# Optimization experiments

Hardware: AMD Instinct MI355X
Metric: run time of the kernel (lower is better)

Reference implementation:

```python
import jax, jax.numpy as jnp
import numpy as np

N, INSIZE, K, D = 512, 512, 64, 16


def setup_inputs() -> dict:
    key = jax.random.key(0)
    k1, k2, k3 = jax.random.split(key, 3)
    x = jax.random.normal(k1, (N, INSIZE), dtype=jnp.float32)
    W = jax.random.normal(k2, (K * D, INSIZE), dtype=jnp.float32) * (1.0 / np.sqrt(INSIZE))
    b = jax.random.normal(k3, (K * D,), dtype=jnp.float32) * 0.01
    return {"x": x, "W": W, "b": b}


def reference(x, W, b):
    # Linear: [N, insize] -> [N, K*D] -> [N, K, D]
    feat = (x @ W.T + b).reshape(-1, K, D)
    n = feat.shape[0]
    # Pairwise L1 distance over D: norm[i, k, j] = sum_d |feat[i,k,d] - feat[j,k,d]|
    # feature [N,K,D,1] vs feature_ [1,K,D,N] in the original broadcast
    diff = jnp.abs(feat[:, :, :, None] - jnp.transpose(feat, (1, 2, 0))[None])  # [N,K,D,N]
    norm = jnp.sum(diff, axis=2)  # [N,K,N]
    # Eraser: suppress self-similarity on the diagonal with a large penalty
    eraser = jnp.eye(n, dtype=feat.dtype)[:, None, :]  # [N,1,N]
    c_b = jnp.exp(-(norm + eraser * 1e6))
    o_b = jnp.sum(c_b, axis=2)  # [N,K]
    return jnp.concatenate((x, o_b), axis=1)  # [N, insize+K]
```

## Files before the change

kernel.cpp:

```cpp
#include <hip/hip_runtime.h>

#define NPTS 512
#define INS  512
#define KDIM 64
#define DDIM 16
#define CDIM (KDIM*DDIM)
#define OUTC (INS + KDIM)

typedef __attribute__((ext_vector_type(4))) float f32x4;
typedef __attribute__((ext_vector_type(8))) short short8v;
typedef __attribute__((ext_vector_type(4))) unsigned short u16x4;
typedef __attribute__((ext_vector_type(8))) unsigned short u16x8;

__device__ __forceinline__ float exp2_fast(float x) {
    return __builtin_amdgcn_exp2f(x);
}

__device__ __forceinline__ unsigned short f2bf_rne(float f) {
    unsigned u = __float_as_uint(f);
    u += 0x7FFF + ((u >> 16) & 1);
    return (unsigned short)(u >> 16);
}
__device__ __forceinline__ float bf2f(unsigned short h) {
    return __uint_as_float(((unsigned)h) << 16);
}

__global__ __launch_bounds__(256) void convert_kernel(
    const float* __restrict__ x, const float* __restrict__ W,
    unsigned short* __restrict__ xh, unsigned short* __restrict__ xl,
    unsigned short* __restrict__ wh, unsigned short* __restrict__ wl)
{
    const int gid = blockIdx.x * 256 + threadIdx.x;
    const float4* src;
    unsigned short *dh, *dl;
    int idx;
    if (gid < NPTS * INS / 4) {
        src = (const float4*)x; idx = gid; dh = xh; dl = xl;
    } else {
        src = (const float4*)W; idx = gid - NPTS * INS / 4; dh = wh; dl = wl;
    }
    float4 v = src[idx];
    u16x4 hv, lv;
    hv[0] = f2bf_rne(v.x); lv[0] = f2bf_rne(v.x - bf2f(hv[0]));
    hv[1] = f2bf_rne(v.y); lv[1] = f2bf_rne(v.y - bf2f(hv[1]));
    hv[2] = f2bf_rne(v.z); lv[2] = f2bf_rne(v.z - bf2f(hv[2]));
    hv[3] = f2bf_rne(v.w); lv[3] = f2bf_rne(v.w - bf2f(hv[3]));
    *(u16x4*)&dh[idx * 4] = hv;
    *(u16x4*)&dl[idx * 4] = lv;
}

#define BM 64
#define BN 64
#define BK 32
#define LDK 40

__global__ __launch_bounds__(256) void gemm_mfma_kernel(
    const unsigned short* __restrict__ xh, const unsigned short* __restrict__ xl,
    const unsigned short* __restrict__ wh, const unsigned short* __restrict__ wl,
    const float* __restrict__ bias,
    float* __restrict__ featT)
{
    __shared__ unsigned short Ah[BM * LDK], Al[BM * LDK];
    __shared__ unsigned short Bh[BN * LDK], Bl[BN * LDK];

    const int tid   = threadIdx.x;
    const int cbase = blockIdx.x * BN;
    const int ibase = blockIdx.y * BM;

    const int lane = tid & 63;
    const int wv   = tid >> 6;
    const int wm   = wv >> 1;
    const int wn   = wv & 1;

    const int srow = tid >> 2;
    const int skg  = tid & 3;
    const size_t gA0 = (size_t)(ibase + srow) * INS + skg * 8;
    const size_t gB0 = (size_t)(cbase + srow) * INS + skg * 8;
    const int    loff = srow * LDK + skg * 8;

    const int frow  = lane & 15;
    const int fg    = lane >> 4;
    const int aoff  = (wm * 32 + frow) * LDK + fg * 8;
    const int boff  = (wn * 32 + frow) * LDK + fg * 8;

    f32x4 acc[2][2] = {};

    u16x8 ra = *(const u16x8*)&xh[gA0];
    u16x8 rl = *(const u16x8*)&xl[gA0];
    u16x8 rb = *(const u16x8*)&wh[gB0];
    u16x8 rc = *(const u16x8*)&wl[gB0];

    for (int kt = 0; kt < INS / BK; ++kt) {
        __syncthreads();
        *(u16x8*)&Ah[loff] = ra;
        *(u16x8*)&Al[loff] = rl;
        *(u16x8*)&Bh[loff] = rb;
        *(u16x8*)&Bl[loff] = rc;
        __syncthreads();
        if (kt + 1 < INS / BK) {
            const size_t o = (size_t)(kt + 1) * BK;
            ra = *(const u16x8*)&xh[gA0 + o];
            rl = *(const u16x8*)&xl[gA0 + o];
            rb = *(const u16x8*)&wh[gB0 + o];
            rc = *(const u16x8*)&wl[gB0 + o];
        }

        short8v ah[2], al[2], bh[2], bl[2];
        #pragma unroll
        for (int f = 0; f < 2; ++f) {
            ah[f] = *(const short8v*)&Ah[aoff + f * 16 * LDK];
            al[f] = *(const short8v*)&Al[aoff + f * 16 * LDK];
            bh[f] = *(const short8v*)&Bh[boff + f * 16 * LDK];
            bl[f] = *(const short8v*)&Bl[boff + f * 16 * LDK];
        }
        #pragma unroll
        for (int m = 0; m < 2; ++m) {
            #pragma unroll
            for (int n = 0; n < 2; ++n) {
                acc[m][n] = __builtin_amdgcn_mfma_f32_16x16x32_bf16(ah[m], bh[n], acc[m][n], 0, 0, 0);
                acc[m][n] = __builtin_amdgcn_mfma_f32_16x16x32_bf16(ah[m], bl[n], acc[m][n], 0, 0, 0);
                acc[m][n] = __builtin_amdgcn_mfma_f32_16x16x32_bf16(al[m], bh[n], acc[m][n], 0, 0, 0);
            }
        }
    }

    const float LOG2E = 1.4426950408889634f;
    const int r0 = (lane >> 4) * 4;
    #pragma unroll
    for (int m = 0; m < 2; ++m) {
        const int i0 = ibase + wm * 32 + m * 16 + r0;
        #pragma unroll
        for (int n = 0; n < 2; ++n) {
            const int c  = cbase + wn * 32 + n * 16 + (lane & 15);
            const float bv = bias[c];
            const int kk = c >> 4;
            const int d  = c & 15;
            float* dst = featT + (size_t)kk * NPTS * DDIM + d;
            #pragma unroll
            for (int r = 0; r < 4; ++r) {
                dst[(size_t)(i0 + r) * DDIM] = (acc[m][n][r] + bv) * LOG2E;
            }
        }
    }
}

__global__ __launch_bounds__(256) void init_out_kernel(
    const float* __restrict__ x, float* __restrict__ out)
{
    const int idx = blockIdx.x * 256 + threadIdx.x;
    const int i  = idx / (OUTC / 4);
    const int j4 = idx - i * (OUTC / 4);
    float4 v;
    if (j4 < INS / 4) {
        v = ((const float4*)x)[i * (INS / 4) + j4];
    } else {
        v = make_float4(-1.0f, -1.0f, -1.0f, -1.0f);
    }
    ((float4*)out)[idx] = v;
}

__global__ __launch_bounds__(256, 4) void pairwise_kernel(
    const float* __restrict__ f0, float* __restrict__ out)
{
    const int k     = blockIdx.x;
    const int itile = blockIdx.y;
    const int jq    = blockIdx.z;

    __shared__ float fj[128 * DDIM];
    __shared__ float part[4][128];

    {
        const size_t base = ((size_t)k * NPTS + jq * 128) * DDIM;
        const float4* s0 = (const float4*)(f0 + base);
        float4* dst = (float4*)fj;
        dst[threadIdx.x]       = s0[threadIdx.x];
        dst[threadIdx.x + 256] = s0[threadIdx.x + 256];
    }

    const int lane = threadIdx.x & 63;
    const int wv   = threadIdx.x >> 6;
    const int i0   = itile * 128 + lane;
    const int i1   = i0 + 64;

    float fi0[16], fi1[16];
    {
        const float4* p0 = (const float4*)(f0 + ((size_t)k * NPTS + i0) * DDIM);
        const float4* p1 = (const float4*)(f0 + ((size_t)k * NPTS + i1) * DDIM);
        #pragma unroll
        for (int q = 0; q < 4; ++q) {
            float4 a = p0[q];
            fi0[q * 4 + 0] = a.x; fi0[q * 4 + 1] = a.y;
            fi0[q * 4 + 2] = a.z; fi0[q * 4 + 3] = a.w;
            float4 b = p1[q];
            fi1[q * 4 + 0] = b.x; fi1[q * 4 + 1] = b.y;
            fi1[q * 4 + 2] = b.z; fi1[q * 4 + 3] = b.w;
        }
    }
    __syncthreads();

    float acc0 = 0.f, acc1 = 0.f;
    const float* fp = fj + wv * 32 * DDIM;
    #pragma unroll 2
    for (int jj = 0; jj < 32; ++jj) {
        const float* p = fp + jj * DDIM;
        float4 q0 = *(const float4*)(p);
        float4 q1 = *(const float4*)(p + 4);
        float4 q2 = *(const float4*)(p + 8);
        float4 q3 = *(const float4*)(p + 12);
        {
            float a0 = fabsf(fi0[0]  - q0.x) + fabsf(fi0[1]  - q0.y)
                     + fabsf(fi0[2]  - q0.z) + fabsf(fi0[3]  - q0.w);
            float a1 = fabsf(fi0[4]  - q1.x) + fabsf(fi0[5]  - q1.y)
                     + fabsf(fi0[6]  - q1.z) + fabsf(fi0[7]  - q1.w);
            float a2 = fabsf(fi0[8]  - q2.x) + fabsf(fi0[9]  - q2.y)
                     + fabsf(fi0[10] - q2.z) + fabsf(fi0[11] - q2.w);
            float a3 = fabsf(fi0[12] - q3.x) + fabsf(fi0[13] - q3.y)
                     + fabsf(fi0[14] - q3.z) + fabsf(fi0[15] - q3.w);
            acc0 += exp2_fast(-((a0 + a1) + (a2 + a3)));
        }
        {
            float b0 = fabsf(fi1[0]  - q0.x) + fabsf(fi1[1]  - q0.y)
                     + fabsf(fi1[2]  - q0.z) + fabsf(fi1[3]  - q0.w);
            float b1 = fabsf(fi1[4]  - q1.x) + fabsf(fi1[5]  - q1.y)
                     + fabsf(fi1[6]  - q1.z) + fabsf(fi1[7]  - q1.w);
            float b2 = fabsf(fi1[8]  - q2.x) + fabsf(fi1[9]  - q2.y)
                     + fabsf(fi1[10] - q2.z) + fabsf(fi1[11] - q2.w);
            float b3 = fabsf(fi1[12] - q3.x) + fabsf(fi1[13] - q3.y)
                     + fabsf(fi1[14] - q3.z) + fabsf(fi1[15] - q3.w);
            acc1 += exp2_fast(-((b0 + b1) + (b2 + b3)));
        }
    }

    part[wv][lane]      = acc0;
    part[wv][lane + 64] = acc1;
    __syncthreads();

    if (threadIdx.x < 128) {
        float s = (part[0][threadIdx.x] + part[1][threadIdx.x])
                + (part[2][threadIdx.x] + part[3][threadIdx.x]);
        const int i = itile * 128 + threadIdx.x;
        atomicAdd(&out[(size_t)i * OUTC + INS + k], s);
    }
}

extern "C" void kernel_launch(void* const* d_in, const int* in_sizes, int n_in,
                              void* d_out, int out_size, void* d_ws, size_t ws_size,
                              hipStream_t stream) {
    const float* x    = (const float*)d_in[0];
    const float* W    = (const float*)d_in[1];
    const float* bias = (const float*)d_in[2];
    float* out = (float*)d_out;

    float* featT = (float*)d_ws;
    unsigned short* xh = (unsigned short*)((char*)d_ws + (size_t)(2 << 20));
    unsigned short* xl = xh + (size_t)NPTS * INS;
    unsigned short* wh = xl + (size_t)NPTS * INS;
    unsigned short* wl = wh + (size_t)CDIM * INS;

    convert_kernel<<<dim3((NPTS * INS / 4 + CDIM * INS / 4) / 256), 256, 0, stream>>>(
        x, W, xh, xl, wh, wl);
    gemm_mfma_kernel<<<dim3(CDIM / BN, NPTS / BM), 256, 0, stream>>>(
        xh, xl, wh, wl, bias, featT);
    init_out_kernel<<<dim3(NPTS * (OUTC / 4) / 256), 256, 0, stream>>>(x, out);
    pairwise_kernel<<<dim3(KDIM, 4, 4), 256, 0, stream>>>(featT, out);
}
```

Measured before the change: 94.77 us.

## Fuse output init into convert, halve GEMM M-tile, drop pairwise atomics

The x-to-output copy moves into the convert kernel as extra blocks, which removes the separate init kernel launch. The GEMM M-tile drops from 64 to 32 rows, doubling the block count to improve occupancy on a small problem. The pairwise kernel now uses 1024-thread blocks covering all 512 j-points and reads j-rows directly from global/L1 instead of staging them in LDS. Because each block now holds the full sum, it writes the result directly and subtracts the diagonal self term (1.0), replacing atomicAdd and the -1 initialization. The risk is heavier per-thread global reads in the inner loop and lower per-CU occupancy with the large blocks.

```diff
diff --git a/kernel.cpp b/kernel.cpp
--- a/kernel.cpp
+++ b/kernel.cpp
@@ -27,29 +27,39 @@
 
 __global__ __launch_bounds__(256) void convert_kernel(
     const float* __restrict__ x, const float* __restrict__ W,
+    float* __restrict__ out,
     unsigned short* __restrict__ xh, unsigned short* __restrict__ xl,
     unsigned short* __restrict__ wh, unsigned short* __restrict__ wl)
 {
-    const int gid = blockIdx.x * 256 + threadIdx.x;
-    const float4* src;
-    unsigned short *dh, *dl;
-    int idx;
-    if (gid < NPTS * INS / 4) {
-        src = (const float4*)x; idx = gid; dh = xh; dl = xl;
+    const int b = blockIdx.x;
+    const int tid = threadIdx.x;
+    if (b < 768) {
+        const int gid = b * 256 + tid;
+        const float4* src;
+        unsigned short *dh, *dl;
+        int idx;
+        if (gid < NPTS * INS / 4) {
+            src = (const float4*)x; idx = gid; dh = xh; dl = xl;
+        } else {
+            src = (const float4*)W; idx = gid - NPTS * INS / 4; dh = wh; dl = wl;
+        }
+        float4 v = src[idx];
+        u16x4 hv, lv;
+        hv[0] = f2bf_rne(v.x); lv[0] = f2bf_rne(v.x - bf2f(hv[0]));
+        hv[1] = f2bf_rne(v.y); lv[1] = f2bf_rne(v.y - bf2f(hv[1]));
+        hv[2] = f2bf_rne(v.z); lv[2] = f2bf_rne(v.z - bf2f(hv[2]));
+        hv[3] = f2bf_rne(v.w); lv[3] = f2bf_rne(v.w - bf2f(hv[3]));
+        *(u16x4*)&dh[idx * 4] = hv;
+        *(u16x4*)&dl[idx * 4] = lv;
     } else {
-        src = (const float4*)W; idx = gid - NPTS * INS / 4; dh = wh; dl = wl;
-    }
-    float4 v = src[idx];
-    u16x4 hv, lv;
-    hv[0] = f2bf_rne(v.x); lv[0] = f2bf_rne(v.x - bf2f(hv[0]));
-    hv[1] = f2bf_rne(v.y); lv[1] = f2bf_rne(v.y - bf2f(hv[1]));
-    hv[2] = f2bf_rne(v.z); lv[2] = f2bf_rne(v.z - bf2f(hv[2]));
-    hv[3] = f2bf_rne(v.w); lv[3] = f2bf_rne(v.w - bf2f(hv[3]));
-    *(u16x4*)&dh[idx * 4] = hv;
-    *(u16x4*)&dl[idx * 4] = lv;
-}
-
-#define BM 64
+        const int idx = (b - 768) * 256 + tid;
+        const int i  = idx >> 7;
+        const int j4 = idx & 127;
+        ((float4*)out)[i * (OUTC / 4) + j4] = ((const float4*)x)[i * (INS / 4) + j4];
+    }
+}
+
+#define BM 32
 #define BN 64
 #define BK 32
 #define LDK 40
@@ -72,120 +82,87 @@
     const int wm   = wv >> 1;
     const int wn   = wv & 1;
 
-    const int srow = tid >> 2;
-    const int skg  = tid & 3;
-    const size_t gA0 = (size_t)(ibase + srow) * INS + skg * 8;
-    const size_t gB0 = (size_t)(cbase + srow) * INS + skg * 8;
-    const int    loff = srow * LDK + skg * 8;
-
-    const int frow  = lane & 15;
-    const int fg    = lane >> 4;
-    const int aoff  = (wm * 32 + frow) * LDK + fg * 8;
-    const int boff  = (wn * 32 + frow) * LDK + fg * 8;
-
-    f32x4 acc[2][2] = {};
-
-    u16x8 ra = *(const u16x8*)&xh[gA0];
-    u16x8 rl = *(const u16x8*)&xl[gA0];
-    u16x8 rb = *(const u16x8*)&wh[gB0];
-    u16x8 rc = *(const u16x8*)&wl[gB0];
+    const int arow = (tid & 127) >> 2;
+    const int brow = tid >> 2;
+    const int kg   = tid & 3;
+    const bool doA = (tid < 128);
+    const size_t gA0 = (size_t)(ibase + arow) * INS + kg * 8;
+    const size_t gB0 = (size_t)(cbase + brow) * INS + kg * 8;
+    const int aloff = arow * LDK + kg * 8;
+    const int bloff = brow * LDK + kg * 8;
+
+    const int frow = lane & 15;
+    const int fg   = lane >> 4;
+    const int aoff = (wm * 16 + frow) * LDK + fg * 8;
+    const int boff = (wn * 32 + frow) * LDK + fg * 8;
+
+    f32x4 acc[2] = {};
+
+    u16x8 rah, ral, rbh, rbl;
+    if (doA) { rah = *(const u16x8*)&xh[gA0]; ral = *(const u16x8*)&xl[gA0]; }
+    rbh = *(const u16x8*)&wh[gB0];
+    rbl = *(const u16x8*)&wl[gB0];
 
     for (int kt = 0; kt < INS / BK; ++kt) {
         __syncthreads();
-        *(u16x8*)&Ah[loff] = ra;
-        *(u16x8*)&Al[loff] = rl;
-        *(u16x8*)&Bh[loff] = rb;
-        *(u16x8*)&Bl[loff] = rc;
+        if (doA) { *(u16x8*)&Ah[aloff] = rah; *(u16x8*)&Al[aloff] = ral; }
+        *(u16x8*)&Bh[bloff] = rbh;
+        *(u16x8*)&Bl[bloff] = rbl;
         __syncthreads();
         if (kt + 1 < INS / BK) {
             const size_t o = (size_t)(kt + 1) * BK;
-            ra = *(const u16x8*)&xh[gA0 + o];
-            rl = *(const u16x8*)&xl[gA0 + o];
-            rb = *(const u16x8*)&wh[gB0 + o];
-            rc = *(const u16x8*)&wl[gB0 + o];
-        }
-
-        short8v ah[2], al[2], bh[2], bl[2];
+            if (doA) { rah = *(const u16x8*)&xh[gA0 + o]; ral = *(const u16x8*)&xl[gA0 + o]; }
+            rbh = *(const u16x8*)&wh[gB0 + o];
+            rbl = *(const u16x8*)&wl[gB0 + o];
+        }
+
+        short8v av_h = *(const short8v*)&Ah[aoff];
+        short8v av_l = *(const short8v*)&Al[aoff];
         #pragma unroll
-        for (int f = 0; f < 2; ++f) {
-            ah[f] = *(const short8v*)&Ah[aoff + f * 16 * LDK];
-            al[f] = *(const short8v*)&Al[aoff + f * 16 * LDK];
-            bh[f] = *(const short8v*)&Bh[boff + f * 16 * LDK];
-            bl[f] = *(const short8v*)&Bl[boff + f * 16 * LDK];
-        }
-        #pragma unroll
-        for (int m = 0; m < 2; ++m) {
-            #pragma unroll
-            for (int n = 0; n < 2; ++n) {
-                acc[m][n] = __builtin_amdgcn_mfma_f32_16x16x32_bf16(ah[m], bh[n], acc[m][n], 0, 0, 0);
-                acc[m][n] = __builtin_amdgcn_mfma_f32_16x16x32_bf16(ah[m], bl[n], acc[m][n], 0, 0, 0);
-                acc[m][n] = __builtin_amdgcn_mfma_f32_16x16x32_bf16(al[m], bh[n], acc[m][n], 0, 0, 0);
-            }
+        for (int n = 0; n < 2; ++n) {
+            short8v bv_h = *(const short8v*)&Bh[boff + n * 16 * LDK];
+            short8v bv_l = *(const short8v*)&Bl[boff + n * 16 * LDK];
+            acc[n] = __builtin_amdgcn_mfma_f32_16x16x32_bf16(av_h, bv_h, acc[n], 0, 0, 0);
+            acc[n] = __builtin_amdgcn_mfma_f32_16x16x32_bf16(av_h, bv_l, acc[n], 0, 0, 0);
+            acc[n] = __builtin_amdgcn_mfma_f32_16x16x32_bf16(av_l, bv_h, acc[n], 0, 0, 0);
         }
     }
 
     const float LOG2E = 1.4426950408889634f;
     const int r0 = (lane >> 4) * 4;
+    const int i0 = ibase + wm * 16 + r0;
     #pragma unroll
-    for (int m = 0; m < 2; ++m) {
-        const int i0 = ibase + wm * 32 + m * 16 + r0;
+    for (int n = 0; n < 2; ++n) {
+        const int c  = cbase + wn * 32 + n * 16 + (lane & 15);
+        const float bv = bias[c];
+        const int kk = c >> 4;
+        const int d  = c & 15;
+        float* dst = featT + (size_t)kk * NPTS * DDIM + d;
         #pragma unroll
-        for (int n = 0; n < 2; ++n) {
-            const int c  = cbase + wn * 32 + n * 16 + (lane & 15);
-            const float bv = bias[c];
-            const int kk = c >> 4;
-            const int d  = c & 15;
-            float* dst = featT + (size_t)kk * NPTS * DDIM + d;
-            #pragma unroll
-            for (int r = 0; r < 4; ++r) {
-                dst[(size_t)(i0 + r) * DDIM] = (acc[m][n][r] + bv) * LOG2E;
-            }
-        }
-    }
-}
-
-__global__ __launch_bounds__(256) void init_out_kernel(
-    const float* __restrict__ x, float* __restrict__ out)
-{
-    const int idx = blockIdx.x * 256 + threadIdx.x;
-    const int i  = idx / (OUTC / 4);
-    const int j4 = idx - i * (OUTC / 4);
-    float4 v;
-    if (j4 < INS / 4) {
-        v = ((const float4*)x)[i * (INS / 4) + j4];
-    } else {
-        v = make_float4(-1.0f, -1.0f, -1.0f, -1.0f);
-    }
-    ((float4*)out)[idx] = v;
-}
-
-__global__ __launch_bounds__(256, 4) void pairwise_kernel(
-    const float* __restrict__ f0, float* __restrict__ out)
+        for (int r = 0; r < 4; ++r) {
+            dst[(size_t)(i0 + r) * DDIM] = (acc[n][r] + bv) * LOG2E;
+        }
+    }
+}
+
+__global__ __launch_bounds__(1024, 4) void pairwise_kernel(
+    const float* __restrict__ f, float* __restrict__ out)
 {
     const int k     = blockIdx.x;
     const int itile = blockIdx.y;
-    const int jq    = blockIdx.z;
-
-    __shared__ float fj[128 * DDIM];
-    __shared__ float part[4][128];
-
-    {
-        const size_t base = ((size_t)k * NPTS + jq * 128) * DDIM;
-        const float4* s0 = (const float4*)(f0 + base);
-        float4* dst = (float4*)fj;
-        dst[threadIdx.x]       = s0[threadIdx.x];
-        dst[threadIdx.x + 256] = s0[threadIdx.x + 256];
-    }
-
-    const int lane = threadIdx.x & 63;
-    const int wv   = threadIdx.x >> 6;
+
+    __shared__ float part[16][128];
+
+    const int tid  = threadIdx.x;
+    const int lane = tid & 63;
+    const int wv   = __builtin_amdgcn_readfirstlane(tid >> 6);
     const int i0   = itile * 128 + lane;
     const int i1   = i0 + 64;
 
     float fi0[16], fi1[16];
     {
-        const float4* p0 = (const float4*)(f0 + ((size_t)k * NPTS + i0) * DDIM);
-        const float4* p1 = (const float4*)(f0 + ((size_t)k * NPTS + i1) * DDIM);
+        const float4* p0 = (const float4*)(f + ((size_t)k * NPTS + i0) * DDIM);
+        const float4* p1 = (const float4*)(f + ((size_t)k * NPTS + i1) * DDIM);
         #pragma unroll
         for (int q = 0; q < 4; ++q) {
             float4 a = p0[q];
@@ -196,13 +173,13 @@
             fi1[q * 4 + 2] = b.z; fi1[q * 4 + 3] = b.w;
         }
     }
-    __syncthreads();
+
+    const float* __restrict__ jrow = f + ((size_t)k * NPTS + wv * 32) * DDIM;
 
     float acc0 = 0.f, acc1 = 0.f;
-    const float* fp = fj + wv * 32 * DDIM;
     #pragma unroll 2
     for (int jj = 0; jj < 32; ++jj) {
-        const float* p = fp + jj * DDIM;
+        const float* p = jrow + jj * DDIM;
         float4 q0 = *(const float4*)(p);
         float4 q1 = *(const float4*)(p + 4);
         float4 q2 = *(const float4*)(p + 8);
@@ -235,11 +212,13 @@
     part[wv][lane + 64] = acc1;
     __syncthreads();
 
-    if (threadIdx.x < 128) {
-        float s = (part[0][threadIdx.x] + part[1][threadIdx.x])
-                + (part[2][threadIdx.x] + part[3][threadIdx.x]);
-        const int i = itile * 128 + threadIdx.x;
-        atomicAdd(&out[(size_t)i * OUTC + INS + k], s);
+    if (tid < 128) {
+        float s = (((part[0][tid]  + part[1][tid])  + (part[2][tid]  + part[3][tid]))
+                +  ((part[4][tid]  + part[5][tid])  + (part[6][tid]  + part[7][tid])))
+                + (((part[8][tid]  + part[9][tid])  + (part[10][tid] + part[11][tid]))
+                +  ((part[12][tid] + part[13][tid]) + (part[14][tid] + part[15][tid])));
+        const int i = itile * 128 + tid;
+        out[(size_t)i * OUTC + INS + k] = s - 1.0f;
     }
 }
 
@@ -257,10 +236,8 @@
     unsigned short* wh = xl + (size_t)NPTS * INS;
     unsigned short* wl = wh + (size_t)CDIM * INS;
 
-    convert_kernel<<<dim3((NPTS * INS / 4 + CDIM * INS / 4) / 256), 256, 0, stream>>>(
-        x, W, xh, xl, wh, wl);
+    convert_kernel<<<dim3(1024), 256, 0, stream>>>(x, W, out, xh, xl, wh, wl);
     gemm_mfma_kernel<<<dim3(CDIM / BN, NPTS / BM), 256, 0, stream>>>(
         xh, xl, wh, wl, bias, featT);
-    init_out_kernel<<<dim3(NPTS * (OUTC / 4) / 256), 256, 0, stream>>>(x, out);
-    pairwise_kernel<<<dim3(KDIM, 4, 4), 256, 0, stream>>>(featT, out);
-}
+    pairwise_kernel<<<dim3(KDIM, 4), 1024, 0, stream>>>(featT, out);
+}
```

Measured after the change: 91.25 us. -3.7%, faster.
